# Performance work log

Hardware: AMD Instinct MI355X
Metric: run time of the kernel (lower is better)

Reference implementation:

```python
import jax, jax.numpy as jnp
import numpy as np

N_NODES = 100000
N_EDGES = 500000
IN_DIM = 16
HEADS = 4
OUT_DIM = 128  # per head; concat=True -> 512 total
NEG_SLOPE = 0.2


def setup_inputs() -> dict:
    key = jax.random.key(0)
    ks = jax.random.split(key, 6)
    node_edge_feat = jax.random.normal(ks[0], (N_NODES, IN_DIM), dtype=jnp.float32)
    node_to_node_index = jax.random.randint(ks[1], (2, N_EDGES), 0, N_NODES, dtype=jnp.int32)
    s = 1.0 / np.sqrt(IN_DIM)
    W_l = jax.random.normal(ks[2], (IN_DIM, HEADS * OUT_DIM), dtype=jnp.float32) * s
    W_r = jax.random.normal(ks[3], (IN_DIM, HEADS * OUT_DIM), dtype=jnp.float32) * s
    b_l = jnp.zeros((HEADS * OUT_DIM,), jnp.float32)
    b_r = jnp.zeros((HEADS * OUT_DIM,), jnp.float32)
    att = jax.random.normal(ks[4], (HEADS, OUT_DIM), dtype=jnp.float32) * (1.0 / np.sqrt(OUT_DIM))
    bias = jnp.zeros((HEADS * OUT_DIM,), jnp.float32)
    return {
        "node_edge_feat": node_edge_feat,
        "node_to_node_index": node_to_node_index,
        "W_l": W_l, "b_l": b_l, "W_r": W_r, "b_r": b_r,
        "att": att, "bias": bias,
    }


def reference(node_edge_feat, node_to_node_index, W_l, b_l, W_r, b_r, att, bias):
    """GATv2Conv forward (eval mode, dropout off), concat=True."""
    N = node_edge_feat.shape[0]
    src = node_to_node_index[0]  # message source j
    dst = node_to_node_index[1]  # aggregation target i
    x_l = (node_edge_feat @ W_l + b_l).reshape(N, HEADS, OUT_DIM)
    x_r = (node_edge_feat @ W_r + b_r).reshape(N, HEADS, OUT_DIM)
    # per-edge GATv2 score: a^T LeakyReLU(x_l[j] + x_r[i])
    m = jax.nn.leaky_relu(x_l[src] + x_r[dst], NEG_SLOPE)  # [E, H, C]
    e = jnp.einsum('ehc,hc->eh', m, att)                   # [E, H]
    # segment softmax over incoming edges of each target node
    emax = jax.lax.stop_gradient(jax.ops.segment_max(e, dst, num_segments=N))[dst]
    ex = jnp.exp(e - emax)
    denom = jax.ops.segment_sum(ex, dst, num_segments=N)[dst]
    alpha = ex / denom                                     # [E, H]
    # scatter-aggregate alpha-weighted source features
    out = jax.ops.segment_sum(alpha[:, :, None] * x_l[src], dst, num_segments=N)
    return out.reshape(N, HEADS * OUT_DIM) + bias
```

## Files before the change

### kernel.cpp

```cpp
#include <hip/hip_runtime.h>
#include <math.h>

#define HEADS 4
#define OUT_DIM 128
#define HC 512
#define IN_DIM 16
#define NEG_SLOPE 0.2f
#define NPB 64

__global__ __launch_bounds__(256) void proj_kernel(
    const float* __restrict__ x,
    const float* __restrict__ Wl, const float* __restrict__ bl,
    const float* __restrict__ Wr, const float* __restrict__ br,
    float* __restrict__ xl, float* __restrict__ xr, int N)
{
    __shared__ float xs[NPB * IN_DIM];
    const int t = threadIdx.x;
    const int c0 = t * 2;

    float wl0[IN_DIM], wl1[IN_DIM], wr0[IN_DIM], wr1[IN_DIM];
#pragma unroll
    for (int k = 0; k < IN_DIM; ++k) {
        float2 a = *(const float2*)&Wl[k * HC + c0];
        wl0[k] = a.x; wl1[k] = a.y;
        float2 b = *(const float2*)&Wr[k * HC + c0];
        wr0[k] = b.x; wr1[k] = b.y;
    }
    const float2 blv = *(const float2*)&bl[c0];
    const float2 brv = *(const float2*)&br[c0];

    const int base = blockIdx.x * NPB;
    if (base >= N) return;
    const int nn = min(NPB, N - base);
    for (int i = t; i < nn * IN_DIM; i += 256) xs[i] = x[base * IN_DIM + i];
    __syncthreads();

    for (int u = 0; u < nn; ++u) {
        const float* xv = &xs[u * IN_DIM];
        float a0 = blv.x, a1 = blv.y, r0 = brv.x, r1 = brv.y;
#pragma unroll
        for (int k = 0; k < IN_DIM; ++k) {
            const float xk = xv[k];
            a0 = fmaf(xk, wl0[k], a0);
            a1 = fmaf(xk, wl1[k], a1);
            r0 = fmaf(xk, wr0[k], r0);
            r1 = fmaf(xk, wr1[k], r1);
        }
        const int n = base + u;
        *(float2*)&xl[(size_t)n * HC + c0] = make_float2(a0, a1);
        *(float2*)&xr[(size_t)n * HC + c0] = make_float2(r0, r1);
    }
}

__global__ __launch_bounds__(256) void hist_kernel(
    const int* __restrict__ idx, int* __restrict__ counts, int E)
{
    const int e = blockIdx.x * 256 + threadIdx.x;
    if (e < E) atomicAdd(&counts[idx[E + e]], 1);
}

__global__ __launch_bounds__(1024) void scan1_kernel(
    const int* __restrict__ counts, int* __restrict__ starts,
    int* __restrict__ blocksums, int N)
{
    __shared__ int sm[1024];
    const int t = threadIdx.x;
    const int g = blockIdx.x * 1024 + t;
    const int v = (g < N) ? counts[g] : 0;
    sm[t] = v;
    __syncthreads();
    for (int o = 1; o < 1024; o <<= 1) {
        const int a = (t >= o) ? sm[t - o] : 0;
        __syncthreads();
        sm[t] += a;
        __syncthreads();
    }
    if (g < N) starts[g] = sm[t] - v;
    if (t == 1023) blocksums[blockIdx.x] = sm[t];
}

__global__ __launch_bounds__(128) void scan2_kernel(int* __restrict__ blocksums, int nb)
{
    __shared__ int sm[128];
    const int t = threadIdx.x;
    const int v = (t < nb) ? blocksums[t] : 0;
    sm[t] = v;
    __syncthreads();
    for (int o = 1; o < 128; o <<= 1) {
        const int a = (t >= o) ? sm[t - o] : 0;
        __syncthreads();
        sm[t] += a;
        __syncthreads();
    }
    if (t < nb) blocksums[t] = sm[t] - v;
}

__global__ __launch_bounds__(256) void scan3_kernel(
    int* __restrict__ starts, const int* __restrict__ blocksums,
    int* __restrict__ cursor, int N)
{
    const int i = blockIdx.x * 256 + threadIdx.x;
    if (i < N) {
        const int s = starts[i] + blocksums[i >> 10];
        starts[i] = s;
        cursor[i] = s;
    }
}

__global__ __launch_bounds__(256) void fill_kernel(
    const int* __restrict__ idx, int* __restrict__ cursor,
    int* __restrict__ esrc, int E)
{
    const int e = blockIdx.x * 256 + threadIdx.x;
    if (e < E) {
        const int dst = idx[E + e];
        const int p = atomicAdd(&cursor[dst], 1);
        esrc[p] = idx[e];
    }
}

__global__ __launch_bounds__(256) void agg_kernel(
    const int* __restrict__ esrc, const int* __restrict__ starts,
    const int* __restrict__ counts,
    const float* __restrict__ xl, const float* __restrict__ xr,
    const float* __restrict__ att, const float* __restrict__ bias,
    float* __restrict__ out, int N)
{
    const int gid = blockIdx.x * 256 + threadIdx.x;
    const int n = gid >> 6;
    if (n >= N) return;
    const int lane = threadIdx.x & 63;

    const float4* xrp = (const float4*)(xr + (size_t)n * HC);
    const float4 b0 = xrp[lane * 2 + 0];
    const float4 b1 = xrp[lane * 2 + 1];
    const float4* atp = (const float4*)att;
    const float4 t0 = atp[lane * 2 + 0];
    const float4 t1 = atp[lane * 2 + 1];

    const int k0  = __builtin_amdgcn_readfirstlane(starts[n]);
    const int deg = __builtin_amdgcn_readfirstlane(counts[n]);

    float4 acc0 = {0.f, 0.f, 0.f, 0.f};
    float4 acc1 = {0.f, 0.f, 0.f, 0.f};
    float den = 0.f;

    float4 n0, n1, c0, c1;
    if (deg > 0) {
        const int s = __builtin_amdgcn_readfirstlane(esrc[k0]);
        const float4* xp = (const float4*)(xl + (size_t)s * HC);
        n0 = xp[lane * 2 + 0];
        n1 = xp[lane * 2 + 1];
    }
    for (int i = 0; i < deg; ++i) {
        c0 = n0; c1 = n1;
        if (i + 1 < deg) {
            const int s = __builtin_amdgcn_readfirstlane(esrc[k0 + i + 1]);
            const float4* xp = (const float4*)(xl + (size_t)s * HC);
            n0 = xp[lane * 2 + 0];
            n1 = xp[lane * 2 + 1];
        }
        float sc = 0.f, z;
        z = c0.x + b0.x; sc = fmaf(t0.x, (z > 0.f ? z : NEG_SLOPE * z), sc);
        z = c0.y + b0.y; sc = fmaf(t0.y, (z > 0.f ? z : NEG_SLOPE * z), sc);
        z = c0.z + b0.z; sc = fmaf(t0.z, (z > 0.f ? z : NEG_SLOPE * z), sc);
        z = c0.w + b0.w; sc = fmaf(t0.w, (z > 0.f ? z : NEG_SLOPE * z), sc);
        z = c1.x + b1.x; sc = fmaf(t1.x, (z > 0.f ? z : NEG_SLOPE * z), sc);
        z = c1.y + b1.y; sc = fmaf(t1.y, (z > 0.f ? z : NEG_SLOPE * z), sc);
        z = c1.z + b1.z; sc = fmaf(t1.z, (z > 0.f ? z : NEG_SLOPE * z), sc);
        z = c1.w + b1.w; sc = fmaf(t1.w, (z > 0.f ? z : NEG_SLOPE * z), sc);
#pragma unroll
        for (int o = 1; o < 16; o <<= 1) sc += __shfl_xor(sc, o);
        const float ex = __expf(sc);
        den += ex;
        acc0.x = fmaf(ex, c0.x, acc0.x);
        acc0.y = fmaf(ex, c0.y, acc0.y);
        acc0.z = fmaf(ex, c0.z, acc0.z);
        acc0.w = fmaf(ex, c0.w, acc0.w);
        acc1.x = fmaf(ex, c1.x, acc1.x);
        acc1.y = fmaf(ex, c1.y, acc1.y);
        acc1.z = fmaf(ex, c1.z, acc1.z);
        acc1.w = fmaf(ex, c1.w, acc1.w);
    }

    const float inv = den > 0.f ? 1.f / den : 0.f;
    const float4* bp = (const float4*)bias;
    const float4 bb0 = bp[lane * 2 + 0];
    const float4 bb1 = bp[lane * 2 + 1];
    float4 o0, o1;
    o0.x = fmaf(acc0.x, inv, bb0.x);
    o0.y = fmaf(acc0.y, inv, bb0.y);
    o0.z = fmaf(acc0.z, inv, bb0.z);
    o0.w = fmaf(acc0.w, inv, bb0.w);
    o1.x = fmaf(acc1.x, inv, bb1.x);
    o1.y = fmaf(acc1.y, inv, bb1.y);
    o1.z = fmaf(acc1.z, inv, bb1.z);
    o1.w = fmaf(acc1.w, inv, bb1.w);
    float4* op = (float4*)(out + (size_t)n * HC);
    op[lane * 2 + 0] = o0;
    op[lane * 2 + 1] = o1;
}

extern "C" void kernel_launch(void* const* d_in, const int* in_sizes, int n_in,
                              void* d_out, int out_size, void* d_ws, size_t ws_size,
                              hipStream_t stream)
{
    const float* x    = (const float*)d_in[0];
    const int*   idx  = (const int*)d_in[1];
    const float* Wl   = (const float*)d_in[2];
    const float* bl   = (const float*)d_in[3];
    const float* Wr   = (const float*)d_in[4];
    const float* br   = (const float*)d_in[5];
    const float* att  = (const float*)d_in[6];
    const float* bias = (const float*)d_in[7];

    const int N = in_sizes[0] / IN_DIM;
    const int E = in_sizes[1] / 2;

    float* xl        = (float*)d_ws;
    float* xr        = xl + (size_t)N * HC;
    int*   counts    = (int*)(xr + (size_t)N * HC);
    int*   starts    = counts + N;
    int*   cursor    = starts + N;
    int*   blocksums = cursor + N;
    int*   esrc      = blocksums + 128;
    float* outf      = (float*)d_out;

    const int nb = (N + 1023) / 1024;

    hipMemsetAsync(counts, 0, (size_t)N * sizeof(int), stream);

    proj_kernel<<<(N + NPB - 1) / NPB, 256, 0, stream>>>(x, Wl, bl, Wr, br, xl, xr, N);

    hist_kernel<<<(E + 255) / 256, 256, 0, stream>>>(idx, counts, E);
    scan1_kernel<<<nb, 1024, 0, stream>>>(counts, starts, blocksums, N);
    scan2_kernel<<<1, 128, 0, stream>>>(blocksums, nb);
    scan3_kernel<<<(N + 255) / 256, 256, 0, stream>>>(starts, blocksums, cursor, N);
    fill_kernel<<<(E + 255) / 256, 256, 0, stream>>>(idx, cursor, esrc, E);

    agg_kernel<<<(N * 64 + 255) / 256, 256, 0, stream>>>(
        esrc, starts, counts, xl, xr, att, bias, outf, N);
}
```

Baseline: 539.1 us.

## Aggregate raw 16-dim inputs and reproject, store projections in fp16, warp-shuffle scan

Because x_l is linear in the input, the weighted sum of x_l rows becomes W_l applied to the weighted sum of raw 16-dim inputs plus the bias. The aggregation kernel now accumulates only 16 floats per head, and a new final kernel applies W_l, b_l and bias to produce the output. The x_l/x_r projections used for the attention scores are stored in fp16 to halve gather bandwidth, at the cost of some precision in the scores. The block scan is rewritten with wave shuffles instead of a shared-memory loop with many barriers. This adds one extra kernel launch and intermediate buffers for the normalised sums and the denominators.

```diff
diff --git a/kernel.cpp b/kernel.cpp
--- a/kernel.cpp
+++ b/kernel.cpp
@@ -1,4 +1,5 @@
 #include <hip/hip_runtime.h>
+#include <hip/hip_fp16.h>
 #include <math.h>
 
 #define HEADS 4
@@ -7,12 +8,13 @@
 #define IN_DIM 16
 #define NEG_SLOPE 0.2f
 #define NPB 64
+#define FNPB 64
 
 __global__ __launch_bounds__(256) void proj_kernel(
     const float* __restrict__ x,
     const float* __restrict__ Wl, const float* __restrict__ bl,
     const float* __restrict__ Wr, const float* __restrict__ br,
-    float* __restrict__ xl, float* __restrict__ xr, int N)
+    __half* __restrict__ xl, __half* __restrict__ xr, int N)
 {
     __shared__ float xs[NPB * IN_DIM];
     const int t = threadIdx.x;
@@ -46,9 +48,9 @@
             r0 = fmaf(xk, wr0[k], r0);
             r1 = fmaf(xk, wr1[k], r1);
         }
-        const int n = base + u;
-        *(float2*)&xl[(size_t)n * HC + c0] = make_float2(a0, a1);
-        *(float2*)&xr[(size_t)n * HC + c0] = make_float2(r0, r1);
+        const size_t n = base + u;
+        *(__half2*)&xl[n * HC + c0] = __floats2half2_rn(a0, a1);
+        *(__half2*)&xr[n * HC + c0] = __floats2half2_rn(r0, r1);
     }
 }
 
@@ -63,20 +65,31 @@
     const int* __restrict__ counts, int* __restrict__ starts,
     int* __restrict__ blocksums, int N)
 {
-    __shared__ int sm[1024];
+    __shared__ int wsum[16];
     const int t = threadIdx.x;
     const int g = blockIdx.x * 1024 + t;
     const int v = (g < N) ? counts[g] : 0;
-    sm[t] = v;
-    __syncthreads();
-    for (int o = 1; o < 1024; o <<= 1) {
-        const int a = (t >= o) ? sm[t - o] : 0;
-        __syncthreads();
-        sm[t] += a;
-        __syncthreads();
-    }
-    if (g < N) starts[g] = sm[t] - v;
-    if (t == 1023) blocksums[blockIdx.x] = sm[t];
+    int xi = v;
+#pragma unroll
+    for (int o = 1; o < 64; o <<= 1) {
+        const int y = __shfl_up(xi, o);
+        if ((t & 63) >= o) xi += y;
+    }
+    if ((t & 63) == 63) wsum[t >> 6] = xi;
+    __syncthreads();
+    if (t < 16) {
+        const int w = wsum[t];
+        int xx = w;
+#pragma unroll
+        for (int o = 1; o < 16; o <<= 1) {
+            const int y = __shfl_up(xx, o);
+            if (t >= o) xx += y;
+        }
+        wsum[t] = xx - w;
+        if (t == 15) blocksums[blockIdx.x] = xx;
+    }
+    __syncthreads();
+    if (g < N) starts[g] = xi - v + wsum[t >> 6];
 }
 
 __global__ __launch_bounds__(128) void scan2_kernel(int* __restrict__ blocksums, int nb)
@@ -119,21 +132,33 @@
     }
 }
 
+__device__ __forceinline__ void h8_to_f(const uint4 u, float4& a, float4& b)
+{
+    const __half2* hp = (const __half2*)&u;
+    const float2 f0 = __half22float2(hp[0]);
+    const float2 f1 = __half22float2(hp[1]);
+    const float2 f2 = __half22float2(hp[2]);
+    const float2 f3 = __half22float2(hp[3]);
+    a = make_float4(f0.x, f0.y, f1.x, f1.y);
+    b = make_float4(f2.x, f2.y, f3.x, f3.y);
+}
+
 __global__ __launch_bounds__(256) void agg_kernel(
     const int* __restrict__ esrc, const int* __restrict__ starts,
     const int* __restrict__ counts,
-    const float* __restrict__ xl, const float* __restrict__ xr,
-    const float* __restrict__ att, const float* __restrict__ bias,
-    float* __restrict__ out, int N)
+    const __half* __restrict__ xl, const __half* __restrict__ xr,
+    const float* __restrict__ xraw, const float* __restrict__ att,
+    float* __restrict__ ynorm, float* __restrict__ denout, int N)
 {
     const int gid = blockIdx.x * 256 + threadIdx.x;
     const int n = gid >> 6;
     if (n >= N) return;
     const int lane = threadIdx.x & 63;
-
-    const float4* xrp = (const float4*)(xr + (size_t)n * HC);
-    const float4 b0 = xrp[lane * 2 + 0];
-    const float4 b1 = xrp[lane * 2 + 1];
+    const int k = lane & 15;
+
+    const uint4 ur = *(const uint4*)(xr + (size_t)n * HC + lane * 8);
+    float4 b0, b1;
+    h8_to_f(ur, b0, b1);
     const float4* atp = (const float4*)att;
     const float4 t0 = atp[lane * 2 + 0];
     const float4 t1 = atp[lane * 2 + 1];
@@ -141,64 +166,91 @@
     const int k0  = __builtin_amdgcn_readfirstlane(starts[n]);
     const int deg = __builtin_amdgcn_readfirstlane(counts[n]);
 
-    float4 acc0 = {0.f, 0.f, 0.f, 0.f};
-    float4 acc1 = {0.f, 0.f, 0.f, 0.f};
-    float den = 0.f;
-
-    float4 n0, n1, c0, c1;
+    float y = 0.f, den = 0.f;
+    uint4 rA = make_uint4(0, 0, 0, 0), rB = make_uint4(0, 0, 0, 0);
+    float xkA = 0.f, xkB = 0.f;
     if (deg > 0) {
         const int s = __builtin_amdgcn_readfirstlane(esrc[k0]);
-        const float4* xp = (const float4*)(xl + (size_t)s * HC);
-        n0 = xp[lane * 2 + 0];
-        n1 = xp[lane * 2 + 1];
+        rA  = *(const uint4*)(xl + (size_t)s * HC + lane * 8);
+        xkA = xraw[s * IN_DIM + k];
+    }
+    if (deg > 1) {
+        const int s = __builtin_amdgcn_readfirstlane(esrc[k0 + 1]);
+        rB  = *(const uint4*)(xl + (size_t)s * HC + lane * 8);
+        xkB = xraw[s * IN_DIM + k];
     }
     for (int i = 0; i < deg; ++i) {
-        c0 = n0; c1 = n1;
-        if (i + 1 < deg) {
-            const int s = __builtin_amdgcn_readfirstlane(esrc[k0 + i + 1]);
-            const float4* xp = (const float4*)(xl + (size_t)s * HC);
-            n0 = xp[lane * 2 + 0];
-            n1 = xp[lane * 2 + 1];
+        const uint4 rc = rA; const float xk = xkA;
+        rA = rB; xkA = xkB;
+        if (i + 2 < deg) {
+            const int s = __builtin_amdgcn_readfirstlane(esrc[k0 + i + 2]);
+            rB  = *(const uint4*)(xl + (size_t)s * HC + lane * 8);
+            xkB = xraw[s * IN_DIM + k];
         }
+        float4 a0, a1;
+        h8_to_f(rc, a0, a1);
         float sc = 0.f, z;
-        z = c0.x + b0.x; sc = fmaf(t0.x, (z > 0.f ? z : NEG_SLOPE * z), sc);
-        z = c0.y + b0.y; sc = fmaf(t0.y, (z > 0.f ? z : NEG_SLOPE * z), sc);
-        z = c0.z + b0.z; sc = fmaf(t0.z, (z > 0.f ? z : NEG_SLOPE * z), sc);
-        z = c0.w + b0.w; sc = fmaf(t0.w, (z > 0.f ? z : NEG_SLOPE * z), sc);
-        z = c1.x + b1.x; sc = fmaf(t1.x, (z > 0.f ? z : NEG_SLOPE * z), sc);
-        z = c1.y + b1.y; sc = fmaf(t1.y, (z > 0.f ? z : NEG_SLOPE * z), sc);
-        z = c1.z + b1.z; sc = fmaf(t1.z, (z > 0.f ? z : NEG_SLOPE * z), sc);
-        z = c1.w + b1.w; sc = fmaf(t1.w, (z > 0.f ? z : NEG_SLOPE * z), sc);
+        z = a0.x + b0.x; sc = fmaf(t0.x, (z > 0.f ? z : NEG_SLOPE * z), sc);
+        z = a0.y + b0.y; sc = fmaf(t0.y, (z > 0.f ? z : NEG_SLOPE * z), sc);
+        z = a0.z + b0.z; sc = fmaf(t0.z, (z > 0.f ? z : NEG_SLOPE * z), sc);
+        z = a0.w + b0.w; sc = fmaf(t0.w, (z > 0.f ? z : NEG_SLOPE * z), sc);
+        z = a1.x + b1.x; sc = fmaf(t1.x, (z > 0.f ? z : NEG_SLOPE * z), sc);
+        z = a1.y + b1.y; sc = fmaf(t1.y, (z > 0.f ? z : NEG_SLOPE * z), sc);
+        z = a1.z + b1.z; sc = fmaf(t1.z, (z > 0.f ? z : NEG_SLOPE * z), sc);
+        z = a1.w + b1.w; sc = fmaf(t1.w, (z > 0.f ? z : NEG_SLOPE * z), sc);
 #pragma unroll
         for (int o = 1; o < 16; o <<= 1) sc += __shfl_xor(sc, o);
         const float ex = __expf(sc);
         den += ex;
-        acc0.x = fmaf(ex, c0.x, acc0.x);
-        acc0.y = fmaf(ex, c0.y, acc0.y);
-        acc0.z = fmaf(ex, c0.z, acc0.z);
-        acc0.w = fmaf(ex, c0.w, acc0.w);
-        acc1.x = fmaf(ex, c1.x, acc1.x);
-        acc1.y = fmaf(ex, c1.y, acc1.y);
-        acc1.z = fmaf(ex, c1.z, acc1.z);
-        acc1.w = fmaf(ex, c1.w, acc1.w);
+        y = fmaf(ex, xk, y);
     }
 
     const float inv = den > 0.f ? 1.f / den : 0.f;
-    const float4* bp = (const float4*)bias;
-    const float4 bb0 = bp[lane * 2 + 0];
-    const float4 bb1 = bp[lane * 2 + 1];
-    float4 o0, o1;
-    o0.x = fmaf(acc0.x, inv, bb0.x);
-    o0.y = fmaf(acc0.y, inv, bb0.y);
-    o0.z = fmaf(acc0.z, inv, bb0.z);
-    o0.w = fmaf(acc0.w, inv, bb0.w);
-    o1.x = fmaf(acc1.x, inv, bb1.x);
-    o1.y = fmaf(acc1.y, inv, bb1.y);
-    o1.z = fmaf(acc1.z, inv, bb1.z);
-    o1.w = fmaf(acc1.w, inv, bb1.w);
-    float4* op = (float4*)(out + (size_t)n * HC);
-    op[lane * 2 + 0] = o0;
-    op[lane * 2 + 1] = o1;
+    ynorm[(size_t)n * 64 + lane] = y * inv;
+    if (k == 0) denout[(size_t)n * 4 + (lane >> 4)] = den;
+}
+
+__global__ __launch_bounds__(256) void final_kernel(
+    const float* __restrict__ ynorm, const float* __restrict__ den,
+    const float* __restrict__ Wl, const float* __restrict__ bl,
+    const float* __restrict__ bias, float* __restrict__ out, int N)
+{
+    __shared__ float ys[FNPB * 64];
+    __shared__ float dsm[FNPB * 4];
+    const int t = threadIdx.x;
+    const int c0 = t * 2;
+    const int h = t >> 6;
+
+    float w0[IN_DIM], w1[IN_DIM];
+#pragma unroll
+    for (int k = 0; k < IN_DIM; ++k) {
+        const float2 a = *(const float2*)&Wl[k * HC + c0];
+        w0[k] = a.x; w1[k] = a.y;
+    }
+    const float blc0 = bl[c0],   blc1 = bl[c0 + 1];
+    const float bsc0 = bias[c0], bsc1 = bias[c0 + 1];
+
+    const int base = blockIdx.x * FNPB;
+    if (base >= N) return;
+    const int nn = min(FNPB, N - base);
+    for (int i = t; i < nn * 16; i += 256)
+        ((float4*)ys)[i] = ((const float4*)(ynorm + (size_t)base * 64))[i];
+    for (int i = t; i < nn * 4; i += 256) dsm[i] = den[(size_t)base * 4 + i];
+    __syncthreads();
+
+    for (int u = 0; u < nn; ++u) {
+        const float* yr = &ys[u * 64 + h * 16];
+        const float g = dsm[u * 4 + h] > 0.f ? 1.f : 0.f;
+        float o0 = fmaf(g, blc0, bsc0);
+        float o1 = fmaf(g, blc1, bsc1);
+#pragma unroll
+        for (int kk = 0; kk < IN_DIM; ++kk) {
+            const float yv = yr[kk];
+            o0 = fmaf(yv, w0[kk], o0);
+            o1 = fmaf(yv, w1[kk], o1);
+        }
+        *(float2*)&out[(size_t)(base + u) * HC + c0] = make_float2(o0, o1);
+    }
 }
 
 extern "C" void kernel_launch(void* const* d_in, const int* in_sizes, int n_in,
@@ -217,20 +269,22 @@
     const int N = in_sizes[0] / IN_DIM;
     const int E = in_sizes[1] / 2;
 
-    float* xl        = (float*)d_ws;
-    float* xr        = xl + (size_t)N * HC;
-    int*   counts    = (int*)(xr + (size_t)N * HC);
-    int*   starts    = counts + N;
-    int*   cursor    = starts + N;
-    int*   blocksums = cursor + N;
-    int*   esrc      = blocksums + 128;
-    float* outf      = (float*)d_out;
+    __half* xl16     = (__half*)d_ws;
+    __half* xr16     = xl16 + (size_t)N * HC;
+    float*  ynorm    = (float*)(xr16 + (size_t)N * HC);
+    float*  den      = ynorm + (size_t)N * 64;
+    int*    counts   = (int*)(den + (size_t)N * 4);
+    int*    starts   = counts + N;
+    int*    cursor   = starts + N;
+    int*    blocksums= cursor + N;
+    int*    esrc     = blocksums + 128;
+    float*  outf     = (float*)d_out;
 
     const int nb = (N + 1023) / 1024;
 
     hipMemsetAsync(counts, 0, (size_t)N * sizeof(int), stream);
 
-    proj_kernel<<<(N + NPB - 1) / NPB, 256, 0, stream>>>(x, Wl, bl, Wr, br, xl, xr, N);
+    proj_kernel<<<(N + NPB - 1) / NPB, 256, 0, stream>>>(x, Wl, bl, Wr, br, xl16, xr16, N);
 
     hist_kernel<<<(E + 255) / 256, 256, 0, stream>>>(idx, counts, E);
     scan1_kernel<<<nb, 1024, 0, stream>>>(counts, starts, blocksums, N);
@@ -239,5 +293,8 @@
     fill_kernel<<<(E + 255) / 256, 256, 0, stream>>>(idx, cursor, esrc, E);
 
     agg_kernel<<<(N * 64 + 255) / 256, 256, 0, stream>>>(
-        esrc, starts, counts, xl, xr, att, bias, outf, N);
-}
+        esrc, starts, counts, xl16, xr16, x, att, ynorm, den, N);
+
+    final_kernel<<<(N + FNPB - 1) / FNPB, 256, 0, stream>>>(
+        ynorm, den, Wl, bl, bias, outf, N);
+}
```

After: 440.6 us. 1.22x faster.
